# Kernel tuning notes

Hardware: AMD Instinct MI355X
Metric: run time of the kernel (lower is better)

The kernel has to match this reference:

```python
import jax, jax.numpy as jnp
import numpy as np
from jax import lax

K = 3          # kernel_size
STRIDE = 1
PAD = 1        # (K-1)//2
C = 64         # channels
GC = 16        # group_channels
G = C // GC    # groups = 4
NS = 1         # new_size = ratio * stride
EPS = 1e-5


def mish(x):
    return x * jnp.tanh(jax.nn.softplus(x))


def setup_inputs() -> dict:
    key = jax.random.key(0)
    ks = jax.random.split(key, 4)
    B, H, W = 2, 256, 256
    c1_in = C * K * 2 + G * K * K      # 420
    c1_out = C * NS * NS // 4          # 16
    return {
        "inputs": jax.random.normal(ks[0], (B, C, H, W), jnp.float32),
        "conv1_w": jax.random.normal(ks[1], (c1_out, c1_in, 1, 1), jnp.float32) * 0.05,
        "conv1_b": jnp.zeros((c1_out,), jnp.float32),
        "conv2_w": jax.random.normal(ks[2], (C // 4, C // 4, 3, 3), jnp.float32) * 0.05,
        "conv2_b": jnp.zeros((C // 4,), jnp.float32),
        "conv3_w": jax.random.normal(ks[3], (G * K * K, C // 4, 1, 1), jnp.float32) * 0.05,
        "conv3_b": jnp.zeros((G * K * K,), jnp.float32),
        "bn_gamma": jnp.ones((c1_out,), jnp.float32),
        "bn_beta": jnp.zeros((c1_out,), jnp.float32),
        "bn_mean": jnp.zeros((c1_out,), jnp.float32),
        "bn_var": jnp.ones((c1_out,), jnp.float32),
    }


def _unfold(x, h, w):
    # torch.nn.Unfold(K, 1, PAD, STRIDE): output channel layout (C, kh, kw)
    xp = jnp.pad(x, ((0, 0), (0, 0), (PAD, PAD), (PAD, PAD)))
    cols = [xp[:, :, ki:ki + (h - 1) * STRIDE + 1:STRIDE,
                     kj:kj + (w - 1) * STRIDE + 1:STRIDE]
            for ki in range(K) for kj in range(K)]
    return jnp.stack(cols, axis=2)  # (b, C, K*K, h, w)


def reference(inputs, conv1_w, conv1_b, conv2_w, conv2_b, conv3_w, conv3_b,
              bn_gamma, bn_beta, bn_mean, bn_var):
    b, _, Wd, Hd = inputs.shape
    h = (Wd + 2 * PAD - K) // STRIDE + 1
    w = (Hd + 2 * PAD - K) // STRIDE + 1
    x = _unfold(inputs, h, w).reshape(b, G, GC, K, K, h, w)
    # multi-axis max pooling over (group_channels, kh, kw)
    m_gc = x.max(axis=2).reshape(b, -1, h, w)  # (b, G*K*K, h, w)
    m_kh = x.max(axis=3).reshape(b, -1, h, w)  # (b, C*K, h, w)
    m_kw = x.max(axis=4).reshape(b, -1, h, w)  # (b, C*K, h, w)
    weight = jnp.concatenate([m_gc, m_kh, m_kw], axis=1)  # (b, 420, h, w)
    # conv1 (1x1) + Mish
    weight = mish(jnp.einsum('bihw,oi->bohw', weight, conv1_w[:, :, 0, 0])
                  + conv1_b[None, :, None, None])                  # (b, 16, h, w)
    c = C // 4
    # rearrange 'b (c n1 n2) h w -> (b h w) c n1 n2'
    wn = weight.reshape(b, c, NS, NS, h, w).transpose(0, 4, 5, 1, 2, 3)
    wn = wn.reshape(b * h * w, c, NS, NS)
    wn = lax.conv_general_dilated(wn, conv2_w, (1, 1), ((1, 1), (1, 1)),
                                  dimension_numbers=('NCHW', 'OIHW', 'NCHW'))
    wn = wn + conv2_b[None, :, None, None]
    # rearrange back '(b h w) c n1 n2 -> b (c n1 n2) h w'
    wn = wn.reshape(b, h, w, c, NS, NS).transpose(0, 3, 4, 5, 1, 2)
    wn = wn.reshape(b, c * NS * NS, h, w)
    # BatchNorm (inference form with running stats)
    scale = bn_gamma / jnp.sqrt(bn_var + EPS)
    wn = wn * scale[None, :, None, None] + (bn_beta - bn_mean * scale)[None, :, None, None]
    weight = weight * mish(wn)
    # conv3 (1x1) -> per-pixel attention logits
    weight = jnp.einsum('bihw,oi->bohw', weight, conv3_w[:, :, 0, 0]) \
             + conv3_b[None, :, None, None]                          # (b, G*K*K, h, w)
    weight = jax.nn.softmax(weight.reshape(b, G, 1, K * K, NS * NS, h, w), axis=3)
    # softmax-weighted patch aggregation
    agg = jnp.sum(x.reshape(b, G, GC, K * K, 1, h, w) * weight, axis=3)  # (b,G,GC,NS^2,h,w)
    # fold with kernel=stride=NS (non-overlapping): pure reshape/transpose
    out = agg.reshape(b, C, NS, NS, h, w).transpose(0, 1, 4, 2, 5, 3)
    return out.reshape(b, C, h * NS, w * NS)
```

## Files before the change

kernel.cpp:

```cpp
#include <hip/hip_runtime.h>
#include <hip/hip_bf16.h>
#include <math.h>

#define Cch 64
#define Hh  256
#define Ww  256
#define HW  (Hh * Ww)

#define WS_WC2  9216
#define WS_SC   9472
#define WS_OFF  9488

typedef __attribute__((ext_vector_type(8))) short bf16x8;
typedef __attribute__((ext_vector_type(4))) float f32x4;

__device__ __forceinline__ float mishf(float x) {
    float e  = __expf(fminf(x, 15.0f));
    float n  = 1.0f + e;
    float n2 = n * n;
    float t  = __fdividef(n2 - 1.0f, n2 + 1.0f);
    return x > 15.0f ? x : x * t;
}

__device__ __forceinline__ unsigned packbf(float a, float b) {
    unsigned short ua = __builtin_bit_cast(unsigned short, __float2bfloat16(a));
    unsigned short ub = __builtin_bit_cast(unsigned short, __float2bfloat16(b));
    return (unsigned)ua | ((unsigned)ub << 16);
}

__device__ __forceinline__ float conv1_wval2(const float* w1, int m, int s,
                                             int q, int j) {
    if (s < 16) {
        int c = 16 * q + s;
        if (j < 3) return w1[m * 420 + 36 + c * 3 + j];
        if (j < 6) return w1[m * 420 + 228 + c * 3 + (j - 3)];
        return 0.0f;
    } else if (s == 16) {
        return w1[m * 420 + q * 9 + j];
    }
    return (j == 0) ? w1[m * 420 + q * 9 + 8] : 0.0f;
}

__global__ __launch_bounds__(256) void prep_kernel(
    const float* __restrict__ w1, const float* __restrict__ w2,
    const float* __restrict__ b2,
    const float* __restrict__ gamma, const float* __restrict__ beta,
    const float* __restrict__ mean,  const float* __restrict__ var,
    float* __restrict__ ws)
{
    unsigned* wsu = (unsigned*)ws;
    const int tid = threadIdx.x;

    for (int idx = tid; idx < 1152; idx += 256) {
        int s = idx >> 6, lane = idx & 63;
        int m = lane & 15, q = lane >> 4;
        unsigned hi[4], lo[4];
        #pragma unroll
        for (int jp = 0; jp < 4; ++jp) {
            float hv[2], lv[2];
            #pragma unroll
            for (int e = 0; e < 2; ++e) {
                float v  = conv1_wval2(w1, m, s, q, jp * 2 + e);
                float hf = __bfloat162float(__float2bfloat16(v));
                hv[e] = hf;
                lv[e] = v - hf;
            }
            hi[jp] = packbf(hv[0], hv[1]);
            lo[jp] = packbf(lv[0], lv[1]);
        }
        int b0 = idx * 8;
        #pragma unroll
        for (int i = 0; i < 4; ++i) { wsu[b0 + i] = hi[i]; wsu[b0 + 4 + i] = lo[i]; }
    }

    for (int idx = tid; idx < 256; idx += 256) {
        int o = idx / 16, i = idx % 16;
        ws[WS_WC2 + idx] = w2[o * 144 + i * 9 + 4];
    }
    if (tid < 16) {
        float sc = gamma[tid] * rsqrtf(var[tid] + 1e-5f);
        ws[WS_SC + tid]  = sc;
        ws[WS_OFF + tid] = b2[tid] * sc + beta[tid] - mean[tid] * sc;
    }
}

#define LDS_FENCE() do {                                             \
    asm volatile("s_waitcnt lgkmcnt(0)" ::: "memory");               \
    __builtin_amdgcn_sched_barrier(0);                               \
} while (0)

#define LOAD9(dst, cb) do {                                          \
    const float* r0_ = (cb) + (size_t)hmc * Ww + w;                  \
    const float* r1_ = (cb) + (size_t)h   * Ww + w;                  \
    const float* r2_ = (cb) + (size_t)hpc * Ww + w;                  \
    (dst)[0] = r0_[offm]; (dst)[1] = r0_[0]; (dst)[2] = r0_[offp];   \
    (dst)[3] = r1_[offm]; (dst)[4] = r1_[0]; (dst)[5] = r1_[offp];   \
    (dst)[6] = r2_[offm]; (dst)[7] = r2_[0]; (dst)[8] = r2_[offp];   \
} while (0)

#define MASK9IP(p) do {                                              \
    (p)[0] = (okhm && okm) ? (p)[0] : 0.0f;                          \
    (p)[1] =  okhm         ? (p)[1] : 0.0f;                          \
    (p)[2] = (okhm && okp) ? (p)[2] : 0.0f;                          \
    (p)[3] =  okm          ? (p)[3] : 0.0f;                          \
    (p)[5] =  okp          ? (p)[5] : 0.0f;                          \
    (p)[6] = (okhp && okm) ? (p)[6] : 0.0f;                          \
    (p)[7] =  okhp         ? (p)[7] : 0.0f;                          \
    (p)[8] = (okhp && okp) ? (p)[8] : 0.0f;                          \
} while (0)

__device__ __forceinline__ float dot4(f32x4 a, f32x4 b) {
    float r = a[0] * b[0];
    r = fmaf(a[1], b[1], r);
    r = fmaf(a[2], b[2], r);
    r = fmaf(a[3], b[3], r);
    return r;
}

__global__ __launch_bounds__(256) void revo_kernel(
    const float* __restrict__ in,
    const float* __restrict__ b1,
    const float* __restrict__ w3, const float* __restrict__ b3,
    const float* __restrict__ ws,
    float* __restrict__ out)
{
    const int tid = threadIdx.x;
    const int t   = tid >> 6;
    const int l   = tid & 63;
    const int q   = l >> 4;
    const int px  = l & 15;

    const int bid     = blockIdx.x;
    const int logical = ((bid & 7) << 8) + (bid >> 3);
    const int wseg = logical & 3;
    const int h    = (logical >> 2) & (Hh - 1);
    const int b    = logical >> 10;
    const int w    = wseg * 64 + t * 16 + px;

    __shared__ f32x4 ldsf[4][16][5];

    const float* base_c = in + ((size_t)b * Cch + 16 * q) * HW;

    const bool okm = (w > 0);
    const bool okp = (w < Ww - 1);
    const int offm = okm ? -1 : 0;
    const int offp = okp ?  1 : 0;

    const int hm = h - 1, hp = h + 1;
    const bool okhm = (hm >= 0), okhp = (hp < Hh);
    const int hmc = okhm ? hm : 0;
    const int hpc = okhp ? hp : Hh - 1;

    const uint4* wa = (const uint4*)ws;

    f32x4 acc = (f32x4){0.f, 0.f, 0.f, 0.f};
    float gmax[9];
    float pT[9], pN[9];

    LOAD9(pT, base_c);
    #pragma unroll
    for (int s = 0; s < 16; ++s) {
        if (s < 15) LOAD9(pN, base_c + (size_t)(s + 1) * HW);
        MASK9IP(pT);
        if (s == 0) {
            #pragma unroll
            for (int k = 0; k < 9; ++k) gmax[k] = pT[k];
        } else {
            #pragma unroll
            for (int k = 0; k < 9; ++k) gmax[k] = fmaxf(gmax[k], pT[k]);
        }
        float mkh0 = fmaxf(fmaxf(pT[0], pT[3]), pT[6]);
        float mkh1 = fmaxf(fmaxf(pT[1], pT[4]), pT[7]);
        float mkh2 = fmaxf(fmaxf(pT[2], pT[5]), pT[8]);
        float mkw0 = fmaxf(fmaxf(pT[0], pT[1]), pT[2]);
        float mkw1 = fmaxf(fmaxf(pT[3], pT[4]), pT[5]);
        float mkw2 = fmaxf(fmaxf(pT[6], pT[7]), pT[8]);

        uint4 bv;
        bv.x = packbf(mkh0, mkh1);
        bv.y = packbf(mkh2, mkw0);
        bv.z = packbf(mkw1, mkw2);
        bv.w = 0u;

        uint4 Ah = wa[(s * 64 + l) * 2];
        uint4 Al = wa[(s * 64 + l) * 2 + 1];
        acc = __builtin_amdgcn_mfma_f32_16x16x32_bf16(
            __builtin_bit_cast(bf16x8, Ah), __builtin_bit_cast(bf16x8, bv),
            acc, 0, 0, 0);
        acc = __builtin_amdgcn_mfma_f32_16x16x32_bf16(
            __builtin_bit_cast(bf16x8, Al), __builtin_bit_cast(bf16x8, bv),
            acc, 0, 0, 0);

        #pragma unroll
        for (int k = 0; k < 9; ++k) pT[k] = pN[k];
    }
    {
        uint4 bv;
        bv.x = packbf(gmax[0], gmax[1]);
        bv.y = packbf(gmax[2], gmax[3]);
        bv.z = packbf(gmax[4], gmax[5]);
        bv.w = packbf(gmax[6], gmax[7]);
        uint4 Ah = wa[(16 * 64 + l) * 2];
        uint4 Al = wa[(16 * 64 + l) * 2 + 1];
        acc = __builtin_amdgcn_mfma_f32_16x16x32_bf16(
            __builtin_bit_cast(bf16x8, Ah), __builtin_bit_cast(bf16x8, bv),
            acc, 0, 0, 0);
        acc = __builtin_amdgcn_mfma_f32_16x16x32_bf16(
            __builtin_bit_cast(bf16x8, Al), __builtin_bit_cast(bf16x8, bv),
            acc, 0, 0, 0);
        uint4 bv2;
        bv2.x = packbf(gmax[8], 0.0f);
        bv2.y = 0u; bv2.z = 0u; bv2.w = 0u;
        uint4 Ah2 = wa[(17 * 64 + l) * 2];
        uint4 Al2 = wa[(17 * 64 + l) * 2 + 1];
        acc = __builtin_amdgcn_mfma_f32_16x16x32_bf16(
            __builtin_bit_cast(bf16x8, Ah2), __builtin_bit_cast(bf16x8, bv2),
            acc, 0, 0, 0);
        acc = __builtin_amdgcn_mfma_f32_16x16x32_bf16(
            __builtin_bit_cast(bf16x8, Al2), __builtin_bit_cast(bf16x8, bv2),
            acc, 0, 0, 0);
    }

    f32x4 b1q = ((const f32x4*)b1)[q];
    f32x4 fp;
    #pragma unroll
    for (int j = 0; j < 4; ++j) fp[j] = mishf(acc[j] + b1q[j]);

    ldsf[t][px][q] = fp;
    LDS_FENCE();
    f32x4 F0 = ldsf[t][px][0], F1 = ldsf[t][px][1],
          F2 = ldsf[t][px][2], F3 = ldsf[t][px][3];
    LDS_FENCE();

    const f32x4* wc2v = (const f32x4*)(ws + WS_WC2);
    f32x4 scq  = ((const f32x4*)(ws + WS_SC))[q];
    f32x4 offq = ((const f32x4*)(ws + WS_OFF))[q];
    f32x4 f2p;
    #pragma unroll
    for (int j = 0; j < 4; ++j) {
        int o = 4 * q + j;
        float a2 = dot4(wc2v[o * 4 + 0], F0) + dot4(wc2v[o * 4 + 1], F1)
                 + dot4(wc2v[o * 4 + 2], F2) + dot4(wc2v[o * 4 + 3], F3);
        f2p[j] = fp[j] * mishf(a2 * scq[j] + offq[j]);
    }

    ldsf[t][px][q] = f2p;
    LDS_FENCE();
    f32x4 G0 = ldsf[t][px][0], G1 = ldsf[t][px][1],
          G2 = ldsf[t][px][2], G3 = ldsf[t][px][3];
    LDS_FENCE();

    const f32x4* w3v = (const f32x4*)w3;
    float att[9];
    {
        float mx = -1e30f;
        #pragma unroll
        for (int k = 0; k < 9; ++k) {
            int row = q * 9 + k;
            float a2 = b3[row];
            a2 += dot4(w3v[row * 4 + 0], G0) + dot4(w3v[row * 4 + 1], G1)
                + dot4(w3v[row * 4 + 2], G2) + dot4(w3v[row * 4 + 3], G3);
            att[k] = a2;
            mx = fmaxf(mx, a2);
        }
        float sum = 0.0f;
        #pragma unroll
        for (int k = 0; k < 9; ++k) { att[k] = __expf(att[k] - mx); sum += att[k]; }
        float inv = __fdividef(1.0f, sum);
        #pragma unroll
        for (int k = 0; k < 9; ++k) att[k] *= inv;
    }

    float* ob = out + (((size_t)b * Cch + 16 * q) * Hh + h) * Ww + w;
    LOAD9(pT, base_c);
    #pragma unroll
    for (int cc = 0; cc < 16; ++cc) {
        if (cc < 15) LOAD9(pN, base_c + (size_t)(cc + 1) * HW);
        float a2 = 0.0f;
        a2 = fmaf((okhm && okm) ? pT[0] : 0.0f, att[0], a2);
        a2 = fmaf( okhm         ? pT[1] : 0.0f, att[1], a2);
        a2 = fmaf((okhm && okp) ? pT[2] : 0.0f, att[2], a2);
        a2 = fmaf( okm          ? pT[3] : 0.0f, att[3], a2);
        a2 = fmaf( pT[4],                       att[4], a2);
        a2 = fmaf( okp          ? pT[5] : 0.0f, att[5], a2);
        a2 = fmaf((okhp && okm) ? pT[6] : 0.0f, att[6], a2);
        a2 = fmaf( okhp         ? pT[7] : 0.0f, att[7], a2);
        a2 = fmaf((okhp && okp) ? pT[8] : 0.0f, att[8], a2);
        ob[(size_t)cc * HW] = a2;
        #pragma unroll
        for (int k = 0; k < 9; ++k) pT[k] = pN[k];
    }
}

extern "C" void kernel_launch(void* const* d_in, const int* in_sizes, int n_in,
                              void* d_out, int out_size, void* d_ws, size_t ws_size,
                              hipStream_t stream) {
    const float* in    = (const float*)d_in[0];
    const float* w1    = (const float*)d_in[1];
    const float* b1    = (const float*)d_in[2];
    const float* w2    = (const float*)d_in[3];
    const float* b2    = (const float*)d_in[4];
    const float* w3    = (const float*)d_in[5];
    const float* b3    = (const float*)d_in[6];
    const float* gamma = (const float*)d_in[7];
    const float* beta  = (const float*)d_in[8];
    const float* mean  = (const float*)d_in[9];
    const float* var   = (const float*)d_in[10];
    float* out = (float*)d_out;
    float* ws  = (float*)d_ws;

    hipLaunchKernelGGL(prep_kernel, dim3(1), dim3(256), 0, stream,
                       w1, w2, b2, gamma, beta, mean, var, ws);

    hipLaunchKernelGGL(revo_kernel, dim3(2048), dim3(256), 0, stream,
                       in, b1, w3, b3, ws, out);
}
```

Baseline: 98.45 us.

## Drop bf16 hi/lo weight split and stage conv1 weights in LDS

Conv1 weights were stored as a bf16 high part plus a bf16 residual, so every step ran two MFMAs. They are now a single bf16 value, which halves the MFMA count and the weight footprint. Each block copies the 18 KB weight table into shared memory once, and the kernel gets a launch-bounds occupancy hint of 4. The cost is lower conv1 precision, a block-wide barrier and copy at kernel start, and more LDS per block.

```diff
diff --git a/kernel.cpp b/kernel.cpp
--- a/kernel.cpp
+++ b/kernel.cpp
@@ -7,9 +7,9 @@
 #define Ww  256
 #define HW  (Hh * Ww)
 
-#define WS_WC2  9216
-#define WS_SC   9472
-#define WS_OFF  9488
+#define WS_WC2  4608
+#define WS_SC   4864
+#define WS_OFF  4880
 
 typedef __attribute__((ext_vector_type(8))) short bf16x8;
 typedef __attribute__((ext_vector_type(4))) float f32x4;
@@ -54,23 +54,12 @@
     for (int idx = tid; idx < 1152; idx += 256) {
         int s = idx >> 6, lane = idx & 63;
         int m = lane & 15, q = lane >> 4;
-        unsigned hi[4], lo[4];
         #pragma unroll
         for (int jp = 0; jp < 4; ++jp) {
-            float hv[2], lv[2];
-            #pragma unroll
-            for (int e = 0; e < 2; ++e) {
-                float v  = conv1_wval2(w1, m, s, q, jp * 2 + e);
-                float hf = __bfloat162float(__float2bfloat16(v));
-                hv[e] = hf;
-                lv[e] = v - hf;
-            }
-            hi[jp] = packbf(hv[0], hv[1]);
-            lo[jp] = packbf(lv[0], lv[1]);
+            float v0 = conv1_wval2(w1, m, s, q, 2 * jp);
+            float v1 = conv1_wval2(w1, m, s, q, 2 * jp + 1);
+            wsu[idx * 4 + jp] = packbf(v0, v1);
         }
-        int b0 = idx * 8;
-        #pragma unroll
-        for (int i = 0; i < 4; ++i) { wsu[b0 + i] = hi[i]; wsu[b0 + 4 + i] = lo[i]; }
     }
 
     for (int idx = tid; idx < 256; idx += 256) {
@@ -117,7 +106,7 @@
     return r;
 }
 
-__global__ __launch_bounds__(256) void revo_kernel(
+__global__ __launch_bounds__(256, 4) void revo_kernel(
     const float* __restrict__ in,
     const float* __restrict__ b1,
     const float* __restrict__ w3, const float* __restrict__ b3,
@@ -137,7 +126,18 @@
     const int b    = logical >> 10;
     const int w    = wseg * 64 + t * 16 + px;
 
+    __shared__ uint4 Alds[1152];
     __shared__ f32x4 ldsf[4][16][5];
+
+    {
+        const uint4* wa = (const uint4*)ws;
+        #pragma unroll
+        for (int i = 0; i < 5; ++i) {
+            int idx = tid + 256 * i;
+            if (idx < 1152) Alds[idx] = wa[idx];
+        }
+    }
+    __syncthreads();
 
     const float* base_c = in + ((size_t)b * Cch + 16 * q) * HW;
 
@@ -150,8 +150,6 @@
     const bool okhm = (hm >= 0), okhp = (hp < Hh);
     const int hmc = okhm ? hm : 0;
     const int hpc = okhp ? hp : Hh - 1;
-
-    const uint4* wa = (const uint4*)ws;
 
     f32x4 acc = (f32x4){0.f, 0.f, 0.f, 0.f};
     float gmax[9];
@@ -182,13 +180,9 @@
         bv.z = packbf(mkw1, mkw2);
         bv.w = 0u;
 
-        uint4 Ah = wa[(s * 64 + l) * 2];
-        uint4 Al = wa[(s * 64 + l) * 2 + 1];
+        uint4 Ah = Alds[s * 64 + l];
         acc = __builtin_amdgcn_mfma_f32_16x16x32_bf16(
             __builtin_bit_cast(bf16x8, Ah), __builtin_bit_cast(bf16x8, bv),
-            acc, 0, 0, 0);
-        acc = __builtin_amdgcn_mfma_f32_16x16x32_bf16(
-            __builtin_bit_cast(bf16x8, Al), __builtin_bit_cast(bf16x8, bv),
             acc, 0, 0, 0);
 
         #pragma unroll
@@ -200,24 +194,16 @@
         bv.y = packbf(gmax[2], gmax[3]);
         bv.z = packbf(gmax[4], gmax[5]);
         bv.w = packbf(gmax[6], gmax[7]);
-        uint4 Ah = wa[(16 * 64 + l) * 2];
-        uint4 Al = wa[(16 * 64 + l) * 2 + 1];
+        uint4 Ah = Alds[16 * 64 + l];
         acc = __builtin_amdgcn_mfma_f32_16x16x32_bf16(
             __builtin_bit_cast(bf16x8, Ah), __builtin_bit_cast(bf16x8, bv),
-            acc, 0, 0, 0);
-        acc = __builtin_amdgcn_mfma_f32_16x16x32_bf16(
-            __builtin_bit_cast(bf16x8, Al), __builtin_bit_cast(bf16x8, bv),
             acc, 0, 0, 0);
         uint4 bv2;
         bv2.x = packbf(gmax[8], 0.0f);
         bv2.y = 0u; bv2.z = 0u; bv2.w = 0u;
-        uint4 Ah2 = wa[(17 * 64 + l) * 2];
-        uint4 Al2 = wa[(17 * 64 + l) * 2 + 1];
+        uint4 Ah2 = Alds[17 * 64 + l];
         acc = __builtin_amdgcn_mfma_f32_16x16x32_bf16(
             __builtin_bit_cast(bf16x8, Ah2), __builtin_bit_cast(bf16x8, bv2),
-            acc, 0, 0, 0);
-        acc = __builtin_amdgcn_mfma_f32_16x16x32_bf16(
-            __builtin_bit_cast(bf16x8, Al2), __builtin_bit_cast(bf16x8, bv2),
             acc, 0, 0, 0);
     }
 
```

Result: slower. 315.6 us (+220.6%).
